# Kernel tuning notes

Measured on AMD Instinct MI355X. Metric: run time of the kernel, lower is better.

## Reference

```python
import jax, jax.numpy as jnp
import numpy as np

LN_EPS = 1e-5      # torch nn.LayerNorm default
NORM_EPS = 1e-12   # torch F.normalize default
EPS = 1e-8         # loss eps


def layer_norm(x, gamma, beta):
    mu = x.mean(axis=-1, keepdims=True)
    var = x.var(axis=-1, keepdims=True)  # biased, matches torch LN
    return (x - mu) * jax.lax.rsqrt(var + LN_EPS) * gamma + beta


def l2norm(x):
    n = jnp.sqrt(jnp.sum(x * x, axis=-1, keepdims=True))
    return x / jnp.maximum(n, NORM_EPS)


def setup_inputs() -> dict:
    key = jax.random.key(0)
    k1, k2, k3 = jax.random.split(key, 3)
    N, B, L, D = 1024, 64, 197, 768
    text_features = jax.random.normal(k1, (N, D), dtype=jnp.float32)
    vision_tokens = jax.random.normal(k2, (B, L, D), dtype=jnp.float32)
    group_map = jnp.sort(jax.random.randint(k3, (N,), 0, B)).astype(jnp.int64)
    ln_gamma = jnp.ones((D,), dtype=jnp.float32)
    ln_beta = jnp.zeros((D,), dtype=jnp.float32)
    log_loss_temp = jnp.array([np.log(0.07)], dtype=jnp.float32)
    return {
        "text_features": text_features,
        "vision_tokens": vision_tokens,
        "group_map": group_map,
        "ln_gamma": ln_gamma,
        "ln_beta": ln_beta,
        "log_loss_temp": log_loss_temp,
    }


def reference(text_features, vision_tokens, group_map, ln_gamma, ln_beta, log_loss_temp):
    D = text_features.shape[-1]
    # shared LayerNorm on both modalities
    tf = layer_norm(text_features, ln_gamma, ln_beta)          # [N, D]
    vt = layer_norm(vision_tokens, ln_gamma, ln_beta)          # [B, L, D]

    # SimilarityLogit, sim_op='dot': scores / sqrt(D), softmax over tokens
    scores = jnp.einsum('nd,bld->bnl', tf, vt) / jnp.sqrt(jnp.float32(D))
    attn = jax.nn.softmax(scores, axis=-1)                     # [B, N, L]
    aggregated = jnp.einsum('bnl,bld->bnd', attn, vt)          # [B, N, D]

    qn = l2norm(tf)                                            # [N, D]
    an = l2norm(aggregated)                                    # [B, N, D]
    logits = jnp.einsum('nd,bnd->nb', qn, an)                  # [N, B] (== [B,N].T)

    # multi-positive NCE loss (row_sum=False, col_sum=False)
    temp = jnp.exp(log_loss_temp)[0]
    scaled = jnp.exp(logits / temp)                            # [N, B]
    N = scaled.shape[0]
    idx = jnp.arange(N)
    pos = scaled[idx, group_map]                               # [N]

    # row loss: pos / sum over images
    row_p = pos / (scaled.sum(axis=1) + EPS)
    row_loss = -jnp.log(row_p + EPS)

    # column loss: pos / (pos + sum of negatives in its column)
    neg_mask = jnp.ones_like(scaled).at[idx, group_map].set(0.0)
    sum_neg = (scaled * neg_mask).sum(axis=0)[group_map]       # [N]
    col_p = pos / (pos + sum_neg + EPS)
    col_loss = -jnp.log(col_p + EPS)

    return (row_loss.mean() + col_loss.mean()) / 2
```

## Files before the change

### kernel.cpp

```cpp
#include <hip/hip_runtime.h>
#include <hip/hip_bf16.h>
#include <math.h>

#define NN 1024
#define BB 64
#define LL 197
#define LP 256
#define LBV 13
#define VROWS 208
#define DD 768

typedef __attribute__((ext_vector_type(8))) short short8;
typedef __attribute__((ext_vector_type(4))) float f32x4;

constexpr float LN_EPS = 1e-5f;
constexpr float NORM_EPS = 1e-12f;
constexpr float EPS = 1e-8f;

__device__ __forceinline__ float waveSum(float v) {
#pragma unroll
    for (int m = 32; m >= 1; m >>= 1) v += __shfl_xor(v, m, 64);
    return v;
}
__device__ __forceinline__ float grpSum(float v) {
#pragma unroll
    for (int m = 8; m >= 1; m >>= 1) v += __shfl_xor(v, m, 64);
    return v;
}
__device__ __forceinline__ float grpMax(float v) {
#pragma unroll
    for (int m = 8; m >= 1; m >>= 1) v = fmaxf(v, __shfl_xor(v, m, 64));
    return v;
}

__device__ __forceinline__ float bf2f(unsigned short u) {
    unsigned int x = ((unsigned int)u) << 16;
    return reinterpret_cast<float&>(x);
}

__device__ __forceinline__ void gl_lds16(const void* g, void* l) {
    __builtin_amdgcn_global_load_lds(
        (const __attribute__((address_space(1))) unsigned int*)g,
        (__attribute__((address_space(3))) unsigned int*)l, 16, 0, 0);
}

__device__ __forceinline__ void raw_barrier() {
    __builtin_amdgcn_sched_barrier(0);
    __builtin_amdgcn_s_barrier();
    __builtin_amdgcn_sched_barrier(0);
}

__global__ __launch_bounds__(256) void ln_kernel(
    const float* __restrict__ x, __hip_bfloat16* __restrict__ y,
    const float* __restrict__ gamma, const float* __restrict__ beta,
    float* __restrict__ qinv) {
    const int row = blockIdx.x;
    const int tid = threadIdx.x;
    const float* xr = x + (size_t)row * DD;
    __hip_bfloat16* yr = y + (size_t)row * DD;

    float v[3];
    float s = 0.f, ss = 0.f;
#pragma unroll
    for (int c = 0; c < 3; c++) {
        float t = xr[tid + 256 * c];
        v[c] = t; s += t; ss += t * t;
    }
    __shared__ float red[8];
    s = waveSum(s); ss = waveSum(ss);
    const int w = tid >> 6;
    if ((tid & 63) == 0) { red[w] = s; red[4 + w] = ss; }
    __syncthreads();
    s = red[0] + red[1] + red[2] + red[3];
    ss = red[4] + red[5] + red[6] + red[7];
    const float mean = s * (1.f / DD);
    const float var = ss * (1.f / DD) - mean * mean;
    const float rs = rsqrtf(var + LN_EPS);

    float q = 0.f;
#pragma unroll
    for (int c = 0; c < 3; c++) {
        const int d = tid + 256 * c;
        float t = (v[c] - mean) * rs * gamma[d] + beta[d];
        __hip_bfloat16 hb = __float2bfloat16(t);
        yr[d] = hb;
        float tb = __bfloat162float(hb);
        q += tb * tb;
    }
    __syncthreads();
    q = waveSum(q);
    if ((tid & 63) == 0) red[w] = q;
    __syncthreads();
    if (tid == 0) {
        float n2 = red[0] + red[1] + red[2] + red[3];
        qinv[row] = 1.f / fmaxf(sqrtf(n2), NORM_EPS);
    }
}

__global__ __launch_bounds__(256) void ln_vis_kernel(
    const float* __restrict__ x, __hip_bfloat16* __restrict__ y,
    const float* __restrict__ gamma, const float* __restrict__ beta) {
    const int id = blockIdx.x;
    const int xcd = id & 7;
    const int k = id >> 3;
    const int bhi = k >> 8;
    const int l = k & 255;
    const int b = xcd + 8 * bhi;
    const int tid = threadIdx.x;
    __hip_bfloat16* yr = y + ((size_t)b * LP + l) * DD;
    if (l >= LL) {
#pragma unroll
        for (int c = 0; c < 3; c++) yr[tid + 256 * c] = __float2bfloat16(0.f);
        return;
    }
    const float* xr = x + ((size_t)b * LL + l) * DD;

    float v[3];
    float s = 0.f, ss = 0.f;
#pragma unroll
    for (int c = 0; c < 3; c++) {
        float t = xr[tid + 256 * c];
        v[c] = t; s += t; ss += t * t;
    }
    __shared__ float red[8];
    s = waveSum(s); ss = waveSum(ss);
    const int w = tid >> 6;
    if ((tid & 63) == 0) { red[w] = s; red[4 + w] = ss; }
    __syncthreads();
    s = red[0] + red[1] + red[2] + red[3];
    ss = red[4] + red[5] + red[6] + red[7];
    const float mean = s * (1.f / DD);
    const float var = ss * (1.f / DD) - mean * mean;
    const float rs = rsqrtf(var + LN_EPS);
#pragma unroll
    for (int c = 0; c < 3; c++) {
        const int d = tid + 256 * c;
        yr[d] = __float2bfloat16((v[c] - mean) * rs * gamma[d] + beta[d]);
    }
}

__global__ __launch_bounds__(256, 2) void gram_kernel(
    const __hip_bfloat16* __restrict__ vt, __hip_bfloat16* __restrict__ G) {
    const int id = blockIdx.x;
    const int xcd = id & 7;
    const int k = id >> 3;
    const int bhi = k >> 3;
    const int rb = k & 7;
    const int b = xcd + 8 * bhi;
    const int n0 = rb * 32;
    const int tid = threadIdx.x, w = tid >> 6, lane = tid & 63;
    const int g = lane >> 4, c = lane & 15;
    const int gsw = (g ^ ((c ^ (c >> 2)) & 3)) * 16;

    __shared__ __align__(16) unsigned char smem[55296];
    const char* vtbc = (const char*)(vt + (size_t)b * LP * DD);

#define GSTAGE(ks, bsel)                                                        \
    {                                                                           \
        const int kb_ = (ks) * 64;                                              \
        _Pragma("unroll")                                                       \
        for (int q_ = 0; q_ < 4; q_++) {                                        \
            const int o_ = q_ * 4096 + tid * 16;                                \
            const int r_ = o_ >> 6;                                             \
            const int sj_ = ((o_ >> 4) & 3) ^ ((r_ ^ (r_ >> 2)) & 3);           \
            gl_lds16(vtbc + (size_t)r_ * 1536 + kb_ + sj_ * 16,                 \
                     smem + (bsel) * 16384 + q_ * 4096 + w * 1024);             \
        }                                                                       \
        if (w < 2) {                                                            \
            const int o_ = tid * 16;                                            \
            const int r_ = o_ >> 6;                                             \
            const int sj_ = ((o_ >> 4) & 3) ^ ((r_ ^ (r_ >> 2)) & 3);           \
            gl_lds16(vtbc + (size_t)(n0 + r_) * 1536 + kb_ + sj_ * 16,          \
                     smem + 49152 + (bsel) * 2048 + w * 1024);                  \
        }                                                                       \
    }

    f32x4 acc[4][2];
#pragma unroll
    for (int i = 0; i < 4; i++)
#pragma unroll
        for (int nb = 0; nb < 2; nb++) acc[i][nb] = {0.f, 0.f, 0.f, 0.f};

    GSTAGE(0, 0);
    GSTAGE(1, 1);
    asm volatile("s_waitcnt vmcnt(4)" ::: "memory");
    raw_barrier();

    for (int ks = 0; ks < 24; ks++) {
        if (ks < 22) GSTAGE(ks + 2, (ks + 2) % 3);
        const unsigned char* vb = smem + (ks % 3) * 16384;
        const unsigned char* tb = smem + 49152 + (ks % 3) * 2048;
        short8 af[2], bf[4];
#pragma unroll
        for (int nb = 0; nb < 2; nb++)
            af[nb] = *(const short8*)(tb + (nb * 16 + c) * 64 + gsw);
#pragma unroll
        for (int i = 0; i < 4; i++)
            bf[i] = *(const short8*)(vb + ((w + 4 * i) * 16 + c) * 64 + gsw);
#pragma unroll
        for (int i = 0; i < 4; i++)
#pragma unroll
            for (int nb = 0; nb < 2; nb++)
                acc[i][nb] = __builtin_amdgcn_mfma_f32_16x16x32_bf16(
                    af[nb], bf[i], acc[i][nb], 0, 0, 0);
        __builtin_amdgcn_sched_barrier(0);
        if (ks < 22) asm volatile("s_waitcnt vmcnt(4)" ::: "memory");
        else         asm volatile("s_waitcnt vmcnt(0)" ::: "memory");
        raw_barrier();
    }
#undef GSTAGE

    __hip_bfloat16* Gb = G + (size_t)b * LP * LP;
#pragma unroll
    for (int i = 0; i < 4; i++) {
        const int col = (w + 4 * i) * 16 + c;
#pragma unroll
        for (int nb = 0; nb < 2; nb++)
#pragma unroll
            for (int r = 0; r < 4; r++)
                Gb[(size_t)(n0 + nb * 16 + g * 4 + r) * LP + col] =
                    __float2bfloat16(acc[i][nb][r]);
    }
}

__global__ __launch_bounds__(256, 3) void score_kernel(
    const __hip_bfloat16* __restrict__ tf, const __hip_bfloat16* __restrict__ vt,
    const float* __restrict__ qinv, __hip_bfloat16* __restrict__ Pbuf,
    float* __restrict__ numq) {
    const int id = blockIdx.x;
    const int xcd = id & 7;
    const int kk = id >> 3;
    const int bhi = kk >> 4;
    const int nt = kk & 15;
    const int b = xcd + 8 * bhi;
    const int n0 = nt * 64;
    const int tid = threadIdx.x, w = tid >> 6, lane = tid & 63;
    const int g = lane >> 4, c = lane & 15;
    const int gsw = (g ^ ((c ^ (c >> 2)) & 3)) * 16;

    __shared__ __align__(16) unsigned char smem[34816];
    float* mx = (float*)smem;
    float* sm = mx + 256;
    float* nm = sm + 256;

    const char* vtbc = (const char*)(vt + (size_t)b * LP * DD);
    const char* tfc = (const char*)(tf + (size_t)n0 * DD);

#define SSTAGE(ks, bsel)                                                        \
    {                                                                           \
        const int kb_ = (ks) * 64;                                              \
        _Pragma("unroll")                                                       \
        for (int q_ = 0; q_ < 3; q_++) {                                        \
            const int o_ = q_ * 4096 + tid * 16;                                \
            const int r_ = o_ >> 6;                                             \
            const int sj_ = ((o_ >> 4) & 3) ^ ((r_ ^ (r_ >> 2)) & 3);           \
            gl_lds16(vtbc + (size_t)r_ * 1536 + kb_ + sj_ * 16,                 \
                     smem + (bsel) * 13312 + q_ * 4096 + w * 1024);             \
        }                                                                       \
        if (lane < 16) {                                                        \
            const int o_ = 12288 + (w * 16 + lane) * 16;                        \
            const int r_ = o_ >> 6;                                             \
            const int sj_ = ((o_ >> 4) & 3) ^ ((r_ ^ (r_ >> 2)) & 3);           \
            gl_lds16(vtbc + (size_t)r_ * 1536 + kb_ + sj_ * 16,                 \
                     smem + (bsel) * 13312 + 12288 + w * 256);                  \
        }                                                                       \
        {                                                                       \
            const int o_ = tid * 16;                                            \
            const int r_ = o_ >> 6;                                             \
            const int sj_ = ((o_ >> 4) & 3) ^ ((r_ ^ (r_ >> 2)) & 3);           \
            gl_lds16(tfc + (size_t)r_ * 1536 + kb_ + sj_ * 16,                  \
                     smem + 26624 + (bsel) * 4096 + w * 1024);                  \
        }                                                                       \
    }

    f32x4 acc[4][4];
#pragma unroll
    for (int i = 0; i < 4; i++)
#pragma unroll
        for (int nb = 0; nb < 4; nb++) acc[i][nb] = {0.f, 0.f, 0.f, 0.f};

    SSTAGE(0, 0);
    SSTAGE(1, 1);
    asm volatile("s_waitcnt vmcnt(5)" ::: "memory");
    raw_barrier();

    for (int ks = 0; ks < 24; ks++) {
        const unsigned char* vb = smem + (ks & 1) * 13312;
        const unsigned char* tb = smem + 26624 + (ks & 1) * 4096;
        short8 af[4];
#pragma unroll
        for (int nb = 0; nb < 4; nb++)
            af[nb] = *(const short8*)(tb + (nb * 16 + c) * 64 + gsw);
#pragma unroll
        for (int i = 0; i < 4; i++) {
            const int lb = w + 4 * i;
            if (lb < LBV) {
                short8 bfv = *(const short8*)(vb + (lb * 16 + c) * 64 + gsw);
#pragma unroll
                for (int nb = 0; nb < 4; nb++)
                    acc[i][nb] = __builtin_amdgcn_mfma_f32_16x16x32_bf16(
                        af[nb], bfv, acc[i][nb], 0, 0, 0);
            }
        }
        raw_barrier();
        if (ks < 22) {
            SSTAGE(ks + 2, ks & 1);
            asm volatile("s_waitcnt vmcnt(5)" ::: "memory");
        } else {
            asm volatile("s_waitcnt vmcnt(0)" ::: "memory");
        }
        raw_barrier();
    }
#undef SSTAGE

    const float inv_sqrtD = 0.0360843918f;
    float mp[4][4];
#pragma unroll
    for (int nb = 0; nb < 4; nb++)
#pragma unroll
        for (int r = 0; r < 4; r++) mp[nb][r] = -1e30f;
#pragma unroll
    for (int i = 0; i < 4; i++) {
        const int l = (w + 4 * i) * 16 + c;
        if (l < LL) {
#pragma unroll
            for (int nb = 0; nb < 4; nb++)
#pragma unroll
                for (int r = 0; r < 4; r++) mp[nb][r] = fmaxf(mp[nb][r], acc[i][nb][r]);
        }
    }
#pragma unroll
    for (int nb = 0; nb < 4; nb++)
#pragma unroll
        for (int r = 0; r < 4; r++) mp[nb][r] = grpMax(mp[nb][r]);
    if (c == 0) {
#pragma unroll
        for (int nb = 0; nb < 4; nb++)
#pragma unroll
            for (int r = 0; r < 4; r++) mx[(nb * 16 + g * 4 + r) * 4 + w] = mp[nb][r];
    }
    __syncthreads();
    float mf[4][4];
#pragma unroll
    for (int nb = 0; nb < 4; nb++)
#pragma unroll
        for (int r = 0; r < 4; r++) {
            const int row = nb * 16 + g * 4 + r;
            mf[nb][r] = fmaxf(fmaxf(mx[row * 4 + 0], mx[row * 4 + 1]),
                              fmaxf(mx[row * 4 + 2], mx[row * 4 + 3]));
        }

    float sp[4][4], np[4][4];
#pragma unroll
    for (int nb = 0; nb < 4; nb++)
#pragma unroll
        for (int r = 0; r < 4; r++) { sp[nb][r] = 0.f; np[nb][r] = 0.f; }
#pragma unroll
    for (int i = 0; i < 4; i++) {
        const int l = (w + 4 * i) * 16 + c;
#pragma unroll
        for (int nb = 0; nb < 4; nb++)
#pragma unroll
            for (int r = 0; r < 4; r++) {
                const float raw = acc[i][nb][r];
                const float p = (l < LL) ? __expf((raw - mf[nb][r]) * inv_sqrtD) : 0.f;
                acc[i][nb][r] = p;
                sp[nb][r] += p;
                np[nb][r] += p * raw;
            }
    }
#pragma unroll
    for (int nb = 0; nb < 4; nb++)
#pragma unroll
        for (int r = 0; r < 4; r++) { sp[nb][r] = grpSum(sp[nb][r]); np[nb][r] = grpSum(np[nb][r]); }
    if (c == 0) {
#pragma unroll
        for (int nb = 0; nb < 4; nb++)
#pragma unroll
            for (int r = 0; r < 4; r++) {
                const int row = nb * 16 + g * 4 + r;
                sm[row * 4 + w] = sp[nb][r];
                nm[row * 4 + w] = np[nb][r];
            }
    }
    __syncthreads();

    float invs[4][4];
#pragma unroll
    for (int nb = 0; nb < 4; nb++)
#pragma unroll
        for (int r = 0; r < 4; r++) {
            const int row = nb * 16 + g * 4 + r;
            const float ssum = sm[row * 4 + 0] + sm[row * 4 + 1] + sm[row * 4 + 2] + sm[row * 4 + 3];
            invs[nb][r] = 1.f / ssum;
        }

    __hip_bfloat16* Pb = Pbuf + ((size_t)b * NN + n0) * LP;
#pragma unroll
    for (int i = 0; i < 4; i++) {
        const int lb = w + 4 * i;
#pragma unroll
        for (int nb = 0; nb < 4; nb++)
#pragma unroll
            for (int r = 0; r < 4; r++)
                Pb[(size_t)(nb * 16 + g * 4 + r) * LP + lb * 16 + c] =
                    __float2bfloat16(acc[i][nb][r] * invs[nb][r]);
    }

    if (tid < 64) {
        const int row = tid;
        const int n = n0 + row;
        const float ssum = sm[row * 4 + 0] + sm[row * 4 + 1] + sm[row * 4 + 2] + sm[row * 4 + 3];
        const float nsum = nm[row * 4 + 0] + nm[row * 4 + 1] + nm[row * 4 + 2] + nm[row * 4 + 3];
        numq[(size_t)n * BB + b] = (nsum / ssum) * qinv[n];
    }
}

__global__ __launch_bounds__(256, 3) void den_kernel(
    const __hip_bfloat16* __restrict__ Pbuf, const __hip_bfloat16* __restrict__ G,
    const float* __restrict__ numq, float* __restrict__ logits) {
    const int id = blockIdx.x;
    const int xcd = id & 7;
    const int kk = id >> 3;
    const int bhi = kk >> 4;
    const int nt = kk & 15;
    const int b = xcd + 8 * bhi;
    const int n0 = nt * 64;
    const int tid = threadIdx.x, w = tid >> 6, lane = tid & 63;
    const int g = lane >> 4, c = lane & 15;
    const int gsw = (g ^ ((c ^ (c >> 2)) & 3)) * 16;

    __shared__ __align__(16) unsigned char smem[34816];
    float* mx = (float*)smem;

    const char* Gbc = (const char*)(G + (size_t)b * LP * LP);
    const char* Pbc = (const char*)(Pbuf + ((size_t)b * NN + n0) * LP);

#define DSTAGE(ks, bsel)                                                        \
    {                                                                           \
        const int kb_ = (ks) * 64;                                              \
        _Pragma("unroll")                                                       \
        for (int q_ = 0; q_ < 3; q_++) {                                        \
            const int o_ = q_ * 4096 + tid * 16;                                \
            const int r_ = o_ >> 6;                                             \
            const int sj_ = ((o_ >> 4) & 3) ^ ((r_ ^ (r_ >> 2)) & 3);           \
            gl_lds16(Gbc + (size_t)r_ * 512 + kb_ + sj_ * 16,                   \
                     smem + (bsel) * 13312 + q_ * 4096 + w * 1024);             \
        }                                                                       \
        if (lane < 16) {                                                        \
            const int o_ = 12288 + (w * 16 + lane) * 16;                        \
            const int r_ = o_ >> 6;                                             \
            const int sj_ = ((o_ >> 4) & 3) ^ ((r_ ^ (r_ >> 2)) & 3);           \
            gl_lds16(Gbc + (size_t)r_ * 512 + kb_ + sj_ * 16,                   \
                     smem + (bsel) * 13312 + 12288 + w * 256);                  \
        }                                                                       \
        {                                                                       \
            const int o_ = tid * 16;                                            \
            const int r_ = o_ >> 6;                                             \
            const int sj_ = ((o_ >> 4) & 3) ^ ((r_ ^ (r_ >> 2)) & 3);           \
            gl_lds16(Pbc + (size_t)r_ * 512 + kb_ + sj_ * 16,                   \
                     smem + 26624 + (bsel) * 4096 + w * 1024);                  \
        }                                                                       \
    }

    f32x4 acc[4][4];
#pragma unroll
    for (int i = 0; i < 4; i++)
#pragma unroll
        for (int nb = 0; nb < 4; nb++) acc[i][nb] = {0.f, 0.f, 0.f, 0.f};

    DSTAGE(0, 0);
    DSTAGE(1, 1);
    asm volatile("s_waitcnt vmcnt(5)" ::: "memory");
    raw_barrier();

    for (int ks = 0; ks < 7; ks++) {
        const unsigned char* vb = smem + (ks & 1) * 13312;
        const unsigned char* tb = smem + 26624 + (ks & 1) * 4096;
        short8 af[4];
#pragma unroll
        for (int nb = 0; nb < 4; nb++)
            af[nb] = *(const short8*)(tb + (nb * 16 + c) * 64 + gsw);
#pragma unroll
        for (int i = 0; i < 4; i++) {
            const int lb = w + 4 * i;
            if (lb < LBV) {
                short8 bfv = *(const short8*)(vb + (lb * 16 + c) * 64 + gsw);
#pragma unroll
                for (int nb = 0; nb < 4; nb++)
                    acc[i][nb] = __builtin_amdgcn_mfma_f32_16x16x32_bf16(
                        af[nb], bfv, acc[i][nb], 0, 0, 0);
            }
        }
        raw_barrier();
        if (ks < 5) {
            DSTAGE(ks + 2, ks & 1);
            asm volatile("s_waitcnt vmcnt(5)" ::: "memory");
        } else {
            asm volatile("s_waitcnt vmcnt(0)" ::: "memory");
        }
        raw_barrier();
    }
#undef DSTAGE

    const short* Pb = (const short*)Pbc;
    float den[4][4];
#pragma unroll
    for (int nb = 0; nb < 4; nb++)
#pragma unroll
        for (int r = 0; r < 4; r++) den[nb][r] = 0.f;
#pragma unroll
    for (int i = 0; i < 4; i++) {
        const int lb = w + 4 * i;
        if (lb < LBV) {
            const int col = lb * 16 + c;
#pragma unroll
            for (int nb = 0; nb < 4; nb++)
#pragma unroll
                for (int r = 0; r < 4; r++) {
                    const float P = bf2f((unsigned short)Pb[(size_t)(nb * 16 + g * 4 + r) * LP + col]);
                    den[nb][r] += P * acc[i][nb][r];
                }
        }
    }

#pragma unroll
    for (int nb = 0; nb < 4; nb++)
#pragma unroll
        for (int r = 0; r < 4; r++) den[nb][r] = grpSum(den[nb][r]);
    __syncthreads();
    if (c == 0) {
#pragma unroll
        for (int nb = 0; nb < 4; nb++)
#pragma unroll
            for (int r = 0; r < 4; r++) mx[(nb * 16 + g * 4 + r) * 4 + w] = den[nb][r];
    }
    __syncthreads();
    if (tid < 64) {
        const int row = tid;
        const int n = n0 + row;
        const float dsum = mx[row * 4 + 0] + mx[row * 4 + 1] + mx[row * 4 + 2] + mx[row * 4 + 3];
        const float dn = fmaxf(sqrtf(fmaxf(dsum, 0.f)), NORM_EPS);
        logits[(size_t)n * BB + b] = numq[(size_t)n * BB + b] / dn;
    }
}

__global__ __launch_bounds__(64) void loss_row_kernel(
    const float* __restrict__ logits, const int* __restrict__ gm,
    const float* __restrict__ logtemp, float* __restrict__ scaled,
    float* __restrict__ posv, float* __restrict__ rowloss) {
    const int n = blockIdx.x;
    const int b = threadIdx.x;
    const float invtemp = 1.f / expf(logtemp[0]);
    const float e = expf(logits[(size_t)n * BB + b] * invtemp);
    scaled[(size_t)n * BB + b] = e;
    const float sum = waveSum(e);
    const int g = gm[n];
    const float pos = __shfl(e, g, 64);
    if (b == 0) {
        posv[n] = pos;
        rowloss[n] = -logf(pos / (sum + EPS) + EPS);
    }
}

__global__ __launch_bounds__(256) void colsum_kernel(
    const float* __restrict__ scaled, const int* __restrict__ gm,
    float* __restrict__ colsum, float* __restrict__ poscol) {
    const int b = blockIdx.x;
    const int tid = threadIdx.x;
    float s = 0.f, p = 0.f;
    for (int n = tid; n < NN; n += 256) {
        const float e = scaled[(size_t)n * BB + b];
        s += e;
        if (gm[n] == b) p += e;
    }
    s = waveSum(s); p = waveSum(p);
    __shared__ float red[8];
    const int w = tid >> 6;
    if ((tid & 63) == 0) { red[w] = s; red[4 + w] = p; }
    __syncthreads();
    if (tid == 0) {
        colsum[b] = red[0] + red[1] + red[2] + red[3];
        poscol[b] = red[4] + red[5] + red[6] + red[7];
    }
}

__global__ __launch_bounds__(1024) void final_kernel(
    const float* __restrict__ posv, const float* __restrict__ rowloss,
    const float* __restrict__ colsum, const float* __restrict__ poscol,
    const int* __restrict__ gm, float* __restrict__ out) {
    const int n = threadIdx.x;
    const int g = gm[n];
    const float pos = posv[n];
    const float sum_neg = colsum[g] - poscol[g];
    const float cl = -logf(pos / (pos + sum_neg + EPS) + EPS);
    float v = rowloss[n] + cl;
    v = waveSum(v);
    __shared__ float red[16];
    if ((n & 63) == 0) red[n >> 6] = v;
    __syncthreads();
    if (n == 0) {
        float s = 0.f;
#pragma unroll
        for (int i = 0; i < 16; i++) s += red[i];
        out[0] = s / (2.f * NN);
    }
}

extern "C" void kernel_launch(void* const* d_in, const int* in_sizes, int n_in,
                              void* d_out, int out_size, void* d_ws, size_t ws_size,
                              hipStream_t stream) {
    const float* text = (const float*)d_in[0];
    const float* vis = (const float*)d_in[1];
    const int* gm = (const int*)d_in[2];
    const float* gamma = (const float*)d_in[3];
    const float* beta = (const float*)d_in[4];
    const float* logtemp = (const float*)d_in[5];
    float* out = (float*)d_out;

    char* w = (char*)d_ws;
    __hip_bfloat16* tf = (__hip_bfloat16*)w;             w += (size_t)NN * DD * 2;
    __hip_bfloat16* vt = (__hip_bfloat16*)w;             w += (size_t)BB * LP * DD * 2;
    __hip_bfloat16* G  = (__hip_bfloat16*)w;             w += (size_t)BB * LP * LP * 2;
    __hip_bfloat16* Pbuf = (__hip_bfloat16*)w;           w += (size_t)BB * NN * LP * 2;
    float* qinv    = (float*)w;  w += (size_t)NN * 4;
    float* numq    = (float*)w;  w += (size_t)NN * BB * 4;
    float* logits  = (float*)w;  w += (size_t)NN * BB * 4;
    float* scaled  = (float*)w;  w += (size_t)NN * BB * 4;
    float* posv    = (float*)w;  w += (size_t)NN * 4;
    float* rowloss = (float*)w;  w += (size_t)NN * 4;
    float* colsum  = (float*)w;  w += (size_t)BB * 4;
    float* poscol  = (float*)w;  w += (size_t)BB * 4;

    ln_kernel<<<NN, 256, 0, stream>>>(text, tf, gamma, beta, qinv);
    ln_vis_kernel<<<BB * LP, 256, 0, stream>>>(vis, vt, gamma, beta);

    score_kernel<<<1024, 256, 0, stream>>>(tf, vt, qinv, Pbuf, numq);
    gram_kernel<<<512, 256, 0, stream>>>(vt, G);
    den_kernel<<<1024, 256, 0, stream>>>(Pbuf, G, numq, logits);

    loss_row_kernel<<<NN, 64, 0, stream>>>(logits, gm, logtemp, scaled, posv, rowloss);
    colsum_kernel<<<BB, 256, 0, stream>>>(scaled, gm, colsum, poscol);
    final_kernel<<<1, 1024, 0, stream>>>(posv, rowloss, colsum, poscol, gm, out);
}
```

Before: 116.4 us.

## Triple-buffer LDS stages in score and den kernels to drop one barrier

Both the score and den GEMM loops move from a double-buffered LDS ring to a triple-buffered one. The next stage's global-to-LDS loads are now issued at the top of each iteration, before the MFMA work on the current buffer, and the barrier that used to sit between compute and the next load is removed. The aim is to overlap load latency with MFMA compute and halve the number of barriers per k-step. In exchange, LDS use grows from about 34 KB to about 52 KB per block, which may limit how many blocks fit on a CU at launch_bounds(256,3).

```diff
diff --git a/kernel.cpp b/kernel.cpp
--- a/kernel.cpp
+++ b/kernel.cpp
@@ -7,7 +7,6 @@
 #define LL 197
 #define LP 256
 #define LBV 13
-#define VROWS 208
 #define DD 768
 
 typedef __attribute__((ext_vector_type(8))) short short8;
@@ -238,7 +237,7 @@
     const int g = lane >> 4, c = lane & 15;
     const int gsw = (g ^ ((c ^ (c >> 2)) & 3)) * 16;
 
-    __shared__ __align__(16) unsigned char smem[34816];
+    __shared__ __align__(16) unsigned char smem[52224];
     float* mx = (float*)smem;
     float* sm = mx + 256;
     float* nm = sm + 256;
@@ -269,7 +268,7 @@
             const int r_ = o_ >> 6;                                             \
             const int sj_ = ((o_ >> 4) & 3) ^ ((r_ ^ (r_ >> 2)) & 3);           \
             gl_lds16(tfc + (size_t)r_ * 1536 + kb_ + sj_ * 16,                  \
-                     smem + 26624 + (bsel) * 4096 + w * 1024);                  \
+                     smem + 39936 + (bsel) * 4096 + w * 1024);                  \
         }                                                                       \
     }
 
@@ -285,8 +284,9 @@
     raw_barrier();
 
     for (int ks = 0; ks < 24; ks++) {
-        const unsigned char* vb = smem + (ks & 1) * 13312;
-        const unsigned char* tb = smem + 26624 + (ks & 1) * 4096;
+        if (ks < 22) SSTAGE(ks + 2, (ks + 2) % 3);
+        const unsigned char* vb = smem + (ks % 3) * 13312;
+        const unsigned char* tb = smem + 39936 + (ks % 3) * 4096;
         short8 af[4];
 #pragma unroll
         for (int nb = 0; nb < 4; nb++)
@@ -302,13 +302,9 @@
                         af[nb], bfv, acc[i][nb], 0, 0, 0);
             }
         }
-        raw_barrier();
-        if (ks < 22) {
-            SSTAGE(ks + 2, ks & 1);
-            asm volatile("s_waitcnt vmcnt(5)" ::: "memory");
-        } else {
-            asm volatile("s_waitcnt vmcnt(0)" ::: "memory");
-        }
+        __builtin_amdgcn_sched_barrier(0);
+        if (ks < 22) asm volatile("s_waitcnt vmcnt(5)" ::: "memory");
+        else         asm volatile("s_waitcnt vmcnt(0)" ::: "memory");
         raw_barrier();
     }
 #undef SSTAGE
@@ -430,7 +426,7 @@
     const int g = lane >> 4, c = lane & 15;
     const int gsw = (g ^ ((c ^ (c >> 2)) & 3)) * 16;
 
-    __shared__ __align__(16) unsigned char smem[34816];
+    __shared__ __align__(16) unsigned char smem[52224];
     float* mx = (float*)smem;
 
     const char* Gbc = (const char*)(G + (size_t)b * LP * LP);
@@ -459,7 +455,7 @@
             const int r_ = o_ >> 6;                                             \
             const int sj_ = ((o_ >> 4) & 3) ^ ((r_ ^ (r_ >> 2)) & 3);           \
             gl_lds16(Pbc + (size_t)r_ * 512 + kb_ + sj_ * 16,                   \
-                     smem + 26624 + (bsel) * 4096 + w * 1024);                  \
+                     smem + 39936 + (bsel) * 4096 + w * 1024);                  \
         }                                                                       \
     }
 
@@ -475,8 +471,9 @@
     raw_barrier();
 
     for (int ks = 0; ks < 7; ks++) {
-        const unsigned char* vb = smem + (ks & 1) * 13312;
-        const unsigned char* tb = smem + 26624 + (ks & 1) * 4096;
+        if (ks < 5) DSTAGE(ks + 2, (ks + 2) % 3);
+        const unsigned char* vb = smem + (ks % 3) * 13312;
+        const unsigned char* tb = smem + 39936 + (ks % 3) * 4096;
         short8 af[4];
 #pragma unroll
         for (int nb = 0; nb < 4; nb++)
@@ -492,13 +489,9 @@
                         af[nb], bfv, acc[i][nb], 0, 0, 0);
             }
         }
-        raw_barrier();
-        if (ks < 5) {
-            DSTAGE(ks + 2, ks & 1);
-            asm volatile("s_waitcnt vmcnt(5)" ::: "memory");
-        } else {
-            asm volatile("s_waitcnt vmcnt(0)" ::: "memory");
-        }
+        __builtin_amdgcn_sched_barrier(0);
+        if (ks < 5) asm volatile("s_waitcnt vmcnt(5)" ::: "memory");
+        else        asm volatile("s_waitcnt vmcnt(0)" ::: "memory");
         raw_barrier();
     }
 #undef DSTAGE
```

Result: no change. 116.6 us (+0.2%).
